# Performance work log

Measured on AMD Instinct MI355X. Metric: run time of the kernel, lower is better.

Reference implementation:

```python
import jax, jax.numpy as jnp
import numpy as np

DEN_LEAKY = 1e-05
NUM_LEAKY = 1e-20


def _chain_objf(xexp, lengths, e_in, e_out, e_pdf, e_prob, leaky, final, coeff):
    """Leaky-HMM forward recursion (pychain forward_backward objective).

    xexp: [B,T,D] exp'd clamped network outputs
    e_*:  edge lists, either shared [E] or per-utterance [B,E]
    leaky/final: [S] or [B,S]
    Returns scalar objf = sum_b log p(X_b | graph_b).
    """
    B, T, D = xexp.shape
    if leaky.ndim == 1:
        leaky = jnp.broadcast_to(leaky[None, :], (B, leaky.shape[0]))
        final = jnp.broadcast_to(final[None, :], (B, final.shape[0]))
    S = leaky.shape[1]
    if e_in.ndim == 1:
        E = e_in.shape[0]
        e_in = jnp.broadcast_to(e_in[None, :], (B, E))
        e_out = jnp.broadcast_to(e_out[None, :], (B, E))
        e_pdf = jnp.broadcast_to(e_pdf[None, :], (B, E))
        e_prob = jnp.broadcast_to(e_prob[None, :], (B, E))
    seg = (e_out + S * jnp.arange(B, dtype=e_out.dtype)[:, None]).ravel()

    # alpha at t=0: mass 1 on start_state (0), plus leaky mass (alpha_sum = 1)
    alpha0 = jnp.zeros((B, S), xexp.dtype).at[:, 0].set(1.0)
    alpha0 = alpha0 + coeff * leaky

    mask_t = jnp.arange(T)[:, None] < lengths[None, :]  # [T,B] ragged frame mask

    def step(carry, inp):
        alpha, logz = carry
        xt, m = inp  # xt: [B,D], m: [B]
        # transition scores: alpha[src] * graph_prob * exp_logit[pdf]
        vals = (jnp.take_along_axis(alpha, e_in, axis=1)
                * e_prob
                * jnp.take_along_axis(xt, e_pdf, axis=1))  # [B,E]
        anew = jax.ops.segment_sum(vals.ravel(), seg, num_segments=B * S).reshape(B, S)
        asum = anew.sum(-1, keepdims=True)  # [B,1] per-frame arbitrary scale
        adash = (anew + coeff * leaky * asum) / asum  # leaky-HMM + renorm
        alpha = jnp.where(m[:, None], adash, alpha)
        logz = logz + jnp.where(m, jnp.log(asum[:, 0]), 0.0)
        return (alpha, logz), None

    (alpha, logz), _ = jax.lax.scan(
        step, (alpha0, jnp.zeros((B,), xexp.dtype)),
        (jnp.transpose(xexp, (1, 0, 2)), mask_t))
    return jnp.sum(logz + jnp.log(jnp.sum(alpha * final, axis=-1)))


def setup_inputs() -> dict:
    key = jax.random.key(0)
    ks = jax.random.split(key, 12)
    B, T, D = 32, 400, 2048
    S_den, E_den = 2000, 60000
    S_num, E_num = 512, 2048
    x = jax.random.normal(ks[0], (B, T, D), dtype=jnp.float32)
    x_lengths = jnp.clip(T - jnp.arange(B, dtype=jnp.int32) * 8, 32, T)  # sorted desc
    den_e_in = jax.random.randint(ks[1], (E_den,), 0, S_den, dtype=jnp.int32)
    den_e_out = jax.random.randint(ks[2], (E_den,), 0, S_den, dtype=jnp.int32)
    den_e_pdf = jax.random.randint(ks[3], (E_den,), 0, D, dtype=jnp.int32)
    den_e_prob = jax.random.uniform(ks[4], (E_den,), dtype=jnp.float32, minval=0.05, maxval=1.0)
    den_leaky = jax.random.uniform(ks[5], (S_den,), dtype=jnp.float32, minval=0.01, maxval=1.0)
    den_final = jax.random.uniform(ks[6], (S_den,), dtype=jnp.float32, minval=0.1, maxval=1.0)
    num_e_in = jax.random.randint(ks[7], (B, E_num), 0, S_num, dtype=jnp.int32)
    num_e_out = jax.random.randint(ks[8], (B, E_num), 0, S_num, dtype=jnp.int32)
    num_e_pdf = jax.random.randint(ks[9], (B, E_num), 0, D, dtype=jnp.int32)
    num_e_prob = jax.random.uniform(ks[10], (B, E_num), dtype=jnp.float32, minval=0.05, maxval=1.0)
    k11, k12 = jax.random.split(ks[11])
    num_leaky = jax.random.uniform(k11, (B, S_num), dtype=jnp.float32, minval=0.01, maxval=1.0)
    num_final = jax.random.uniform(k12, (B, S_num), dtype=jnp.float32, minval=0.1, maxval=1.0)
    return {"x": x, "x_lengths": x_lengths,
            "den_e_in": den_e_in, "den_e_out": den_e_out, "den_e_pdf": den_e_pdf,
            "den_e_prob": den_e_prob, "den_leaky": den_leaky, "den_final": den_final,
            "num_e_in": num_e_in, "num_e_out": num_e_out, "num_e_pdf": num_e_pdf,
            "num_e_prob": num_e_prob, "num_leaky": num_leaky, "num_final": num_final}


def reference(x, x_lengths, den_e_in, den_e_out, den_e_pdf, den_e_prob, den_leaky,
              den_final, num_e_in, num_e_out, num_e_pdf, num_e_prob, num_leaky,
              num_final):
    xexp = jnp.exp(jnp.clip(x, -30.0, 30.0))
    den_objf = _chain_objf(xexp, x_lengths, den_e_in, den_e_out, den_e_pdf,
                           den_e_prob, den_leaky, den_final, DEN_LEAKY)
    num_objf = _chain_objf(xexp, x_lengths, num_e_in, num_e_out, num_e_pdf,
                           num_e_prob, num_leaky, num_final, NUM_LEAKY)
    objf = -(num_objf - den_objf)
    return objf / x_lengths.sum().astype(x.dtype)
```

## Files before the change

kernel.cpp:

```cpp
#include <hip/hip_runtime.h>
#include <math.h>

#define B_SZ   32
#define T_SZ   400
#define D_SZ   2048
#define S_DEN  2000
#define E_DEN  60000
#define S_NUM  512
#define E_NUM  2048
#define DEN_C  1e-5f
#define NUM_C  1e-20f

#define P_CH   8
#define NTHR   512
#define EPT    16
#define EPC    8192

#define REC_OFF     0u
#define ANEWG_OFF   0u
#define PACK_OFF    960000u
#define ROWPTR_OFF  1484288u
#define CNT_OFF     1492352u
#define CUR_OFF     1500352u
#define SROW_OFF    1508352u
#define RSPLIT_OFF  1524736u
#define PSUM_OFF    1524800u
#define CTR_OFF     1528896u
#define XCD_OFF     1530944u
#define TOTD_OFF    1531968u
#define TOTN_OFF    1532096u
#define WS_BYTES    1532224u

__device__ __forceinline__ float expclip(float v) {
    return __expf(fminf(fmaxf(v, -30.f), 30.f));
}
__device__ __forceinline__ float ldf_agent(const float* p) {
    return __hip_atomic_load(p, __ATOMIC_RELAXED, __HIP_MEMORY_SCOPE_AGENT);
}
__device__ __forceinline__ int ldi_agent(const int* p) {
    return __hip_atomic_load(p, __ATOMIC_RELAXED, __HIP_MEMORY_SCOPE_AGENT);
}
__device__ __forceinline__ void stf_agent(float* p, float v) {
    __hip_atomic_store(p, v, __ATOMIC_RELAXED, __HIP_MEMORY_SCOPE_AGENT);
}
__device__ __forceinline__ void sti_agent(int* p, int v) {
    __hip_atomic_store(p, v, __ATOMIC_RELAXED, __HIP_MEMORY_SCOPE_AGENT);
}

__global__ void prep_init(char* ws) {
    int tid = threadIdx.x;
    int* cnt = (int*)(ws + CNT_OFF);
    int* cur = (int*)(ws + CUR_OFF);
    for (int i = tid; i < S_DEN; i += 256) { cnt[i] = 0; cur[i] = 0; }
    int* ctr = (int*)(ws + CTR_OFF);
    for (int i = tid; i < B_SZ * 16; i += 256) ctr[i] = 0;
    int* xcd = (int*)(ws + XCD_OFF);
    if (tid < B_SZ * 8) xcd[tid] = 0;
}

__global__ void prep_hist(const int* __restrict__ e_out, char* ws) {
    int e = blockIdx.x * blockDim.x + threadIdx.x;
    if (e < E_DEN) atomicAdd((int*)(ws + CNT_OFF) + e_out[e], 1);
}

__global__ __launch_bounds__(1024) void prep_scan(char* ws) {
    __shared__ int sb[2][2048];
    const int* cnt = (const int*)(ws + CNT_OFF);
    int* rowp = (int*)(ws + ROWPTR_OFF);
    int tid = threadIdx.x;
    for (int i = tid; i < 2048; i += 1024) sb[0][i] = (i < S_DEN) ? cnt[i] : 0;
    __syncthreads();
    int cur = 0;
    for (int d = 1; d < 2048; d <<= 1) {
        for (int i = tid; i < 2048; i += 1024)
            sb[1 - cur][i] = sb[cur][i] + ((i >= d) ? sb[cur][i - d] : 0);
        __syncthreads();
        cur ^= 1;
    }
    if (tid == 0) rowp[0] = 0;
    for (int i = tid; i < S_DEN; i += 1024) rowp[i + 1] = sb[cur][i];
    __syncthreads();
    if (tid == 0) {
        int* rs = (int*)(ws + RSPLIT_OFF);
        rs[0] = 0; rs[P_CH] = S_DEN;
        for (int p = 1; p < P_CH; ++p) {
            int target = (E_DEN / P_CH) * p;
            int lo = 0, hi = S_DEN;
            while (lo < hi) {
                int mid = (lo + hi) >> 1;
                int v = (mid == 0) ? 0 : sb[cur][mid - 1];
                if (v >= target) hi = mid; else lo = mid + 1;
            }
            rs[p] = lo;
        }
    }
}

__global__ void prep_scatter(const int* __restrict__ e_in, const int* __restrict__ e_out,
                             const int* __restrict__ e_pdf, const float* __restrict__ e_prob,
                             char* ws) {
    int e = blockIdx.x * blockDim.x + threadIdx.x;
    if (e >= E_DEN) return;
    const int* rowp = (const int*)(ws + ROWPTR_OFF);
    int* cur = (int*)(ws + CUR_OFF);
    int4* recs = (int4*)(ws + REC_OFF);
    int o = e_out[e];
    int pos = rowp[o] + atomicAdd(&cur[o], 1);
    int4 r;
    r.x = e_in[e]; r.y = e_pdf[e];
    r.z = __float_as_int(e_prob[e]);
    r.w = o;
    recs[pos] = r;
}

__global__ void prep_pack(char* ws) {
    int slot = blockIdx.x * blockDim.x + threadIdx.x;
    if (slot >= P_CH * EPC) return;
    int p = slot >> 13;
    int k = slot & (EPC - 1);
    const int* rowp = (const int*)(ws + ROWPTR_OFF);
    const int* rs = (const int*)(ws + RSPLIT_OFF);
    int ebase = rowp[rs[p]], eend = rowp[rs[p + 1]];
    uint2* pk = (uint2*)(ws + PACK_OFF);
    int idx = ebase + k;
    uint2 val;
    int myrow;
    if (idx < eend) {
        const int4* r4 = (const int4*)(ws + REC_OFF);
        int4 r = r4[idx];
        myrow = r.w;
        int nxt = (idx + 1 < eend) ? r4[idx + 1].w : myrow;
        unsigned d = (unsigned)(nxt - myrow);
        if (d > 1023u) d = 1023u;
        val = make_uint2((unsigned)r.x | ((unsigned)r.y << 11) | (d << 22),
                         (unsigned)r.z);
    } else {
        val = make_uint2(0u, 0u);
        myrow = rs[p];
    }
    pk[slot] = val;
    if ((k & (EPT - 1)) == 0)
        ((int*)(ws + SROW_OFF))[(p << 9) + (k >> 4)] = myrow;
}

__global__ __launch_bounds__(NTHR, 2) void chain_fwd6(
    const float* __restrict__ x, const int* __restrict__ lengths,
    const float* __restrict__ den_leaky, const float* __restrict__ den_final,
    const int* __restrict__ num_in, const int* __restrict__ num_out,
    const int* __restrict__ num_pdf, const float* __restrict__ num_prob,
    const float* __restrict__ num_leaky, const float* __restrict__ num_final,
    char* __restrict__ ws)
{
    __shared__ float alpha[2048];
    __shared__ float xrow[2048];
    __shared__ float anew[2048];
    __shared__ float nalpha[S_NUM];
    __shared__ float nanew[S_NUM];
    __shared__ float red[24];
    __shared__ int sSame;
    extern __shared__ float dynpad[];
    const int tid = threadIdx.x;
    if (lengths[0] == -12345) dynpad[tid] = 1.f;

    const int b = blockIdx.x & (B_SZ - 1);
    const int p = blockIdx.x >> 5;
    const bool isNum = (p == 0);
    const int len = lengths[b];
    const float* xb = x + (size_t)b * T_SZ * D_SZ;
    const int* rs = (const int*)(ws + RSPLIT_OFF);
    const int rlo = rs[p], rhi = rs[p + 1];
    float* anewg = (float*)(ws + ANEWG_OFF) + ((size_t)(b << 1) << 11);
    float* psumg = (float*)(ws + PSUM_OFF);
    int* ctr = (int*)(ws + CTR_OFF) + (b << 4);
    int* xcdArr = (int*)(ws + XCD_OFF);

    int myxcc = 0;
    asm volatile("s_getreg_b32 %0, hwreg(HW_REG_XCC_ID)" : "=s"(myxcc));
    if (tid == 0) {
        sti_agent(&xcdArr[(b << 3) + p], myxcc + 1);
        asm volatile("s_waitcnt vmcnt(0)" ::: "memory");
        __hip_atomic_fetch_add(ctr + 1, 1, __ATOMIC_RELAXED, __HIP_MEMORY_SCOPE_AGENT);
    }
    if (tid < 64) {
        int gd = 0;
        while (ldi_agent(ctr + 1) < P_CH) {
            __builtin_amdgcn_s_sleep(2);
            if (++gd > (1 << 16)) break;
        }
        int v = (tid < 8) ? ldi_agent(&xcdArr[(b << 3) + tid]) : -1;
        int v0 = __shfl(v, 0, 64);
        bool eq = (tid < 8) ? (v == v0 && v != 0) : true;
        unsigned long long m = __ballot(eq);
        if (tid == 0) sSame = (~m == 0ULL) ? 1 : 0;
    }

    float lc[4], fc[4];
    #pragma unroll
    for (int i = 0; i < 4; ++i) {
        int s = tid + (i << 9);
        lc[i] = (s < S_DEN) ? DEN_C * den_leaky[s] : 0.f;
        fc[i] = (s < S_DEN) ? den_final[s] : 0.f;
    }
    #pragma unroll
    for (int i = 0; i < 4; ++i) {
        int s = tid + (i << 9);
        alpha[s] = lc[i] + ((s == 0) ? 1.f : 0.f);
        anew[s] = 0.f;
        xrow[s] = expclip(xb[s]);
    }

    float nlk = 0.f, nfn = 0.f, nlogz = 0.f;
    int nein[4], neout[4], nepdf[4]; float neprb[4];
    if (isNum) {
        nlk = num_leaky[(b << 9) + tid];
        nfn = num_final[(b << 9) + tid];
        #pragma unroll
        for (int k = 0; k < 4; ++k) {
            int e = (b << 11) + tid + (k << 9);
            nein[k] = num_in[e]; neout[k] = num_out[e];
            nepdf[k] = num_pdf[e]; neprb[k] = num_prob[e];
        }
        nalpha[tid] = NUM_C * nlk + ((tid == 0) ? 1.f : 0.f);
        nanew[tid] = 0.f;
    }

    const uint4* __restrict__ pk4 = (const uint4*)(ws + PACK_OFF);
    const int qb = (p << 12) + (tid << 3);
    const uint4 c0 = pk4[qb + 0], c1 = pk4[qb + 1], c2 = pk4[qb + 2], c3 = pk4[qb + 3];
    const uint4 c4 = pk4[qb + 4], c5 = pk4[qb + 5], c6 = pk4[qb + 6], c7 = pk4[qb + 7];
    const int row0 = ((const int*)(ws + SROW_OFF))[(p << 9) + tid];
    float logz = 0.f;
    __syncthreads();
    const bool fastSt = (sSame != 0);

    for (int t = 0; t < len; ++t) {
        const int par = t & 1;
        const int tn = (t + 1 < len) ? t + 1 : t;
        const float* xq = xb + (size_t)tn * D_SZ;
        const float xn0 = xq[tid], xn1 = xq[tid + 512];
        const float xn2 = xq[tid + 1024], xn3 = xq[tid + 1536];

        float acc = 0.f, psum = 0.f;
        int row = row0;
        {
            const unsigned w[16] = {c0.x, c0.z, c1.x, c1.z, c2.x, c2.z, c3.x, c3.z,
                                    c4.x, c4.z, c5.x, c5.z, c6.x, c6.z, c7.x, c7.z};
            const unsigned pr[16] = {c0.y, c0.w, c1.y, c1.w, c2.y, c2.w, c3.y, c3.w,
                                     c4.y, c4.w, c5.y, c5.w, c6.y, c6.w, c7.y, c7.w};
            float av[16], xv[16];
            #pragma unroll
            for (int i = 0; i < 16; ++i) av[i] = alpha[w[i] & 2047u];
            #pragma unroll
            for (int i = 0; i < 16; ++i) xv[i] = xrow[(w[i] >> 11) & 2047u];
            #pragma unroll
            for (int i = 0; i < 16; ++i) {
                acc = __fmaf_rn(av[i] * __uint_as_float(pr[i]), xv[i], acc);
                const unsigned d = w[i] >> 22;
                if (d) { psum += acc; atomicAdd(&anew[row], acc); acc = 0.f; row += (int)d; }
            }
        }
        psum += acc;
        if (acc != 0.f) atomicAdd(&anew[row], acc);
        #pragma unroll
        for (int o = 32; o > 0; o >>= 1) psum += __shfl_down(psum, o, 64);
        if ((tid & 63) == 0) red[tid >> 6] = psum;
        __syncthreads();

        float* ag = anewg + (par << 11);
        const int pidx = ((b << 1) | par) << 4;
        if (tid == 0) {
            float bs = red[0]+red[1]+red[2]+red[3]+red[4]+red[5]+red[6]+red[7];
            if (fastSt) psumg[pidx + p] = bs;
            else        stf_agent(&psumg[pidx + p], bs);
        }
        if (fastSt) {
            for (int r = rlo + tid; r < rhi; r += NTHR) { ag[r] = anew[r]; anew[r] = 0.f; }
        } else {
            for (int r = rlo + tid; r < rhi; r += NTHR) { stf_agent(&ag[r], anew[r]); anew[r] = 0.f; }
        }
        asm volatile("s_waitcnt vmcnt(0)" ::: "memory");
        if ((tid & 63) == 0)
            __hip_atomic_fetch_add(ctr, 1, __ATOMIC_RELAXED, __HIP_MEMORY_SCOPE_AGENT);

        if (isNum) {
            #pragma unroll
            for (int k = 0; k < 4; ++k) {
                float v = nalpha[nein[k]] * neprb[k] * xrow[nepdf[k]];
                atomicAdd(&nanew[neout[k]], v);
            }
            __syncthreads();
            float ps = nanew[tid];
            #pragma unroll
            for (int o = 32; o > 0; o >>= 1) ps += __shfl_down(ps, o, 64);
            if ((tid & 63) == 0) red[8 + (tid >> 6)] = ps;
        }

        xrow[tid]        = expclip(xn0);
        xrow[tid + 512]  = expclip(xn1);
        xrow[tid + 1024] = expclip(xn2);
        xrow[tid + 1536] = expclip(xn3);

        if (tid < 64) {
            const int target = (P_CH * (NTHR / 64)) * (t + 1);
            int gd = 0;
            while (ldi_agent(ctr) < target) {
                __builtin_amdgcn_s_sleep(1);
                if (++gd > (1 << 15)) break;
            }
            if (tid < 8) red[16 + tid] = ldf_agent(&psumg[pidx + tid]);
        }
        __syncthreads();

        const float asum = red[16]+red[17]+red[18]+red[19]
                         + red[20]+red[21]+red[22]+red[23];
        const float inv = 1.f / asum;
        #pragma unroll
        for (int i = 0; i < 4; ++i) {
            const int s = tid + (i << 9);
            float an = (s < S_DEN) ? ldf_agent(&ag[s]) : 0.f;
            alpha[s] = __fmaf_rn(an, inv, lc[i]);
        }
        logz += logf(asum);
        if (isNum) {
            const float nasum = red[8]+red[9]+red[10]+red[11]
                              + red[12]+red[13]+red[14]+red[15];
            nalpha[tid] = __fmaf_rn(NUM_C * nlk, nasum, nanew[tid]) * (1.f / nasum);
            nanew[tid] = 0.f;
            nlogz += logf(nasum);
        }
        __syncthreads();
    }

    if (isNum) {
        float fs = alpha[tid] * fc[0] + alpha[tid + 512] * fc[1]
                 + alpha[tid + 1024] * fc[2] + alpha[tid + 1536] * fc[3];
        #pragma unroll
        for (int o = 32; o > 0; o >>= 1) fs += __shfl_down(fs, o, 64);
        if ((tid & 63) == 0) red[tid >> 6] = fs;
        __syncthreads();
        if (tid == 0) {
            float tot = red[0]+red[1]+red[2]+red[3]+red[4]+red[5]+red[6]+red[7];
            ((float*)(ws + TOTD_OFF))[b] = logz + logf(tot);
        }
        __syncthreads();
        float nfs = nalpha[tid] * nfn;
        #pragma unroll
        for (int o = 32; o > 0; o >>= 1) nfs += __shfl_down(nfs, o, 64);
        if ((tid & 63) == 0) red[tid >> 6] = nfs;
        __syncthreads();
        if (tid == 0) {
            float tot = red[0]+red[1]+red[2]+red[3]+red[4]+red[5]+red[6]+red[7];
            ((float*)(ws + TOTN_OFF))[b] = nlogz + logf(tot);
        }
    }
}

__global__ void combine2(const char* __restrict__ ws, const int* __restrict__ lengths,
                         float* __restrict__ out) {
    const float* totd = (const float*)(ws + TOTD_OFF);
    const float* totn = (const float*)(ws + TOTN_OFF);
    int tid = threadIdx.x;
    float v = 0.f, l = 0.f;
    if (tid < B_SZ) { v = totd[tid] - totn[tid]; l = (float)lengths[tid]; }
    #pragma unroll
    for (int o = 32; o > 0; o >>= 1) { v += __shfl_down(v, o, 64); l += __shfl_down(l, o, 64); }
    if (tid == 0) out[0] = v / l;
}

__global__ __launch_bounds__(1024) void chain_fwd_kernel(
    const float* __restrict__ x, const int* __restrict__ lengths,
    const int* __restrict__ den_in, const int* __restrict__ den_out,
    const int* __restrict__ den_pdf, const float* __restrict__ den_prob,
    const float* __restrict__ den_leaky, const float* __restrict__ den_final,
    const int* __restrict__ num_in, const int* __restrict__ num_out,
    const int* __restrict__ num_pdf, const float* __restrict__ num_prob,
    const float* __restrict__ num_leaky, const float* __restrict__ num_final,
    float* __restrict__ part)
{
    __shared__ float xrow[D_SZ];
    __shared__ float alpha[S_DEN];
    __shared__ float anew[S_DEN];
    __shared__ float red[17];
    const int tid = threadIdx.x;
    const int nthr = 1024;
    const bool is_den = blockIdx.x < B_SZ;
    const int b = blockIdx.x & (B_SZ - 1);
    int S, E;
    const int *e_in, *e_out, *e_pdf;
    const float *e_prob, *leaky, *fin;
    float coeff;
    if (is_den) {
        S = S_DEN; E = E_DEN;
        e_in = den_in; e_out = den_out; e_pdf = den_pdf; e_prob = den_prob;
        leaky = den_leaky; fin = den_final; coeff = DEN_C;
    } else {
        S = S_NUM; E = E_NUM;
        e_in = num_in + b * E_NUM; e_out = num_out + b * E_NUM;
        e_pdf = num_pdf + b * E_NUM; e_prob = num_prob + b * E_NUM;
        leaky = num_leaky + b * S_NUM; fin = num_final + b * S_NUM;
        coeff = NUM_C;
    }
    const int len = lengths[b];
    const float* xb = x + (size_t)b * T_SZ * D_SZ;
    for (int s = tid; s < S; s += nthr)
        alpha[s] = coeff * leaky[s] + (s == 0 ? 1.0f : 0.0f);
    float logz = 0.0f;
    for (int t = 0; t < len; ++t) {
        for (int s = tid; s < S; s += nthr) anew[s] = 0.0f;
        const float* xt = xb + (size_t)t * D_SZ;
        for (int d = tid; d < D_SZ; d += nthr)
            xrow[d] = __expf(fminf(fmaxf(xt[d], -30.0f), 30.0f));
        __syncthreads();
        for (int e = tid; e < E; e += nthr) {
            float v = alpha[e_in[e]] * e_prob[e] * xrow[e_pdf[e]];
            atomicAdd(&anew[e_out[e]], v);
        }
        __syncthreads();
        float ps = 0.0f;
        for (int s = tid; s < S; s += nthr) ps += anew[s];
        #pragma unroll
        for (int off = 32; off > 0; off >>= 1) ps += __shfl_down(ps, off, 64);
        if ((tid & 63) == 0) red[tid >> 6] = ps;
        __syncthreads();
        if (tid < 64) {
            float v = (tid < 16) ? red[tid] : 0.0f;
            #pragma unroll
            for (int off = 8; off > 0; off >>= 1) v += __shfl_down(v, off, 64);
            if (tid == 0) red[16] = v;
        }
        __syncthreads();
        const float asum = red[16];
        const float inv = 1.0f / asum;
        for (int s = tid; s < S; s += nthr)
            alpha[s] = (anew[s] + coeff * leaky[s] * asum) * inv;
        logz += logf(asum);
        __syncthreads();
    }
    float fs = 0.0f;
    for (int s = tid; s < S; s += nthr) fs += alpha[s] * fin[s];
    #pragma unroll
    for (int off = 32; off > 0; off >>= 1) fs += __shfl_down(fs, off, 64);
    if ((tid & 63) == 0) red[tid >> 6] = fs;
    __syncthreads();
    if (tid < 64) {
        float v = (tid < 16) ? red[tid] : 0.0f;
        #pragma unroll
        for (int off = 8; off > 0; off >>= 1) v += __shfl_down(v, off, 64);
        if (tid == 0) part[blockIdx.x] = logz + logf(v);
    }
}

__global__ void combine_kernel(const float* __restrict__ part,
                               const int* __restrict__ lengths,
                               float* __restrict__ out)
{
    int tid = threadIdx.x;
    float v = 0.0f, l = 0.0f;
    if (tid < B_SZ) { v = part[tid] - part[B_SZ + tid]; l = (float)lengths[tid]; }
    #pragma unroll
    for (int off = 32; off > 0; off >>= 1) { v += __shfl_down(v, off, 64); l += __shfl_down(l, off, 64); }
    if (tid == 0) out[0] = v / l;
}

extern "C" void kernel_launch(void* const* d_in, const int* in_sizes, int n_in,
                              void* d_out, int out_size, void* d_ws, size_t ws_size,
                              hipStream_t stream)
{
    const float* x          = (const float*)d_in[0];
    const int*   lengths    = (const int*)  d_in[1];
    const int*   den_in_p   = (const int*)  d_in[2];
    const int*   den_out_p  = (const int*)  d_in[3];
    const int*   den_pdf_p  = (const int*)  d_in[4];
    const float* den_prob_p = (const float*)d_in[5];
    const float* den_leaky  = (const float*)d_in[6];
    const float* den_final  = (const float*)d_in[7];
    const int*   num_in_p   = (const int*)  d_in[8];
    const int*   num_out_p  = (const int*)  d_in[9];
    const int*   num_pdf_p  = (const int*)  d_in[10];
    const float* num_prob_p = (const float*)d_in[11];
    const float* num_leaky  = (const float*)d_in[12];
    const float* num_final  = (const float*)d_in[13];

    if (ws_size >= WS_BYTES) {
        char* ws = (char*)d_ws;
        hipLaunchKernelGGL(prep_init, dim3(1), dim3(256), 0, stream, ws);
        hipLaunchKernelGGL(prep_hist, dim3((E_DEN + 255) / 256), dim3(256), 0, stream,
                           den_out_p, ws);
        hipLaunchKernelGGL(prep_scan, dim3(1), dim3(1024), 0, stream, ws);
        hipLaunchKernelGGL(prep_scatter, dim3((E_DEN + 255) / 256), dim3(256), 0, stream,
                           den_in_p, den_out_p, den_pdf_p, den_prob_p, ws);
        hipLaunchKernelGGL(prep_pack, dim3((P_CH * EPC + 255) / 256), dim3(256), 0, stream, ws);
        hipLaunchKernelGGL(chain_fwd6, dim3(P_CH * B_SZ), dim3(NTHR), 57344, stream,
                           x, lengths, den_leaky, den_final,
                           num_in_p, num_out_p, num_pdf_p, num_prob_p,
                           num_leaky, num_final, ws);
        hipLaunchKernelGGL(combine2, dim3(1), dim3(64), 0, stream,
                           ws, lengths, (float*)d_out);
    } else {
        float* part = (float*)d_ws;
        hipLaunchKernelGGL(chain_fwd_kernel, dim3(2 * B_SZ), dim3(1024), 0, stream,
                           x, lengths,
                           den_in_p, den_out_p, den_pdf_p, den_prob_p, den_leaky, den_final,
                           num_in_p, num_out_p, num_pdf_p, num_prob_p, num_leaky, num_final,
                           part);
        hipLaunchKernelGGL(combine_kernel, dim3(1), dim3(64), 0, stream,
                           part, lengths, (float*)d_out);
    }
}
```

Measured before the change: 2.710 ms.

## Replace global per-batch counter barrier with per-chunk flags and wave-local row gathers

Each block now publishes a per-chunk progress flag once all its waves have stored their anew rows, instead of every wave incrementing one shared global counter. Each wave then waits only on the flag of the chunk whose rows it gathers, loads those rows and computes their partial sum. The frame sum therefore comes from the gathered alpha values, and the separate per-block psum exchange goes away. The leaky term moves to a shared array, and the dynamic shared padding shrinks to keep occupancy the same. This cuts contention on the global atomic and overlaps the waits across waves, at the cost of more complex synchronisation and a wave-to-chunk mapping that relies on eight waves matching eight chunks.

```diff
diff --git a/kernel.cpp b/kernel.cpp
--- a/kernel.cpp
+++ b/kernel.cpp
@@ -24,12 +24,12 @@
 #define CUR_OFF     1500352u
 #define SROW_OFF    1508352u
 #define RSPLIT_OFF  1524736u
-#define PSUM_OFF    1524800u
-#define CTR_OFF     1528896u
-#define XCD_OFF     1530944u
-#define TOTD_OFF    1531968u
-#define TOTN_OFF    1532096u
-#define WS_BYTES    1532224u
+#define FLAG_OFF    1524800u
+#define CTR_OFF     1541184u
+#define XCD_OFF     1543232u
+#define TOTD_OFF    1544256u
+#define TOTN_OFF    1544384u
+#define WS_BYTES    1544512u
 
 __device__ __forceinline__ float expclip(float v) {
     return __expf(fminf(fmaxf(v, -30.f), 30.f));
@@ -52,6 +52,8 @@
     int* cnt = (int*)(ws + CNT_OFF);
     int* cur = (int*)(ws + CUR_OFF);
     for (int i = tid; i < S_DEN; i += 256) { cnt[i] = 0; cur[i] = 0; }
+    int* flags = (int*)(ws + FLAG_OFF);
+    for (int i = tid; i < B_SZ * 8 * 16; i += 256) flags[i] = 0;
     int* ctr = (int*)(ws + CTR_OFF);
     for (int i = tid; i < B_SZ * 16; i += 256) ctr[i] = 0;
     int* xcd = (int*)(ws + XCD_OFF);
@@ -143,7 +145,7 @@
         ((int*)(ws + SROW_OFF))[(p << 9) + (k >> 4)] = myrow;
 }
 
-__global__ __launch_bounds__(NTHR, 2) void chain_fwd6(
+__global__ __launch_bounds__(NTHR, 2) void chain_fwd7(
     const float* __restrict__ x, const int* __restrict__ lengths,
     const float* __restrict__ den_leaky, const float* __restrict__ den_final,
     const int* __restrict__ num_in, const int* __restrict__ num_out,
@@ -154,12 +156,16 @@
     __shared__ float alpha[2048];
     __shared__ float xrow[2048];
     __shared__ float anew[2048];
+    __shared__ float slc[2048];
     __shared__ float nalpha[S_NUM];
     __shared__ float nanew[S_NUM];
-    __shared__ float red[24];
-    __shared__ int sSame;
+    __shared__ float red[16];
+    __shared__ int   lcnt;
+    __shared__ int   sSame;
     extern __shared__ float dynpad[];
     const int tid = threadIdx.x;
+    const int wid = tid >> 6;
+    const int lane = tid & 63;
     if (lengths[0] == -12345) dynpad[tid] = 1.f;
 
     const int b = blockIdx.x & (B_SZ - 1);
@@ -169,10 +175,15 @@
     const float* xb = x + (size_t)b * T_SZ * D_SZ;
     const int* rs = (const int*)(ws + RSPLIT_OFF);
     const int rlo = rs[p], rhi = rs[p + 1];
+    const int rloW = rs[wid], rhiW = rs[wid + 1];
     float* anewg = (float*)(ws + ANEWG_OFF) + ((size_t)(b << 1) << 11);
-    float* psumg = (float*)(ws + PSUM_OFF);
+    int* flags = (int*)(ws + FLAG_OFF);
     int* ctr = (int*)(ws + CTR_OFF) + (b << 4);
     int* xcdArr = (int*)(ws + XCD_OFF);
+    int* myflag = &flags[((b << 3) + p) << 4];
+    int* wflag  = &flags[((b << 3) + wid) << 4];
+
+    if (tid == 0) lcnt = 0;
 
     int myxcc = 0;
     asm volatile("s_getreg_b32 %0, hwreg(HW_REG_XCC_ID)" : "=s"(myxcc));
@@ -194,17 +205,14 @@
         if (tid == 0) sSame = (~m == 0ULL) ? 1 : 0;
     }
 
-    float lc[4], fc[4];
+    float fc[4];
     #pragma unroll
     for (int i = 0; i < 4; ++i) {
         int s = tid + (i << 9);
-        lc[i] = (s < S_DEN) ? DEN_C * den_leaky[s] : 0.f;
+        float lv = (s < S_DEN) ? DEN_C * den_leaky[s] : 0.f;
+        slc[s] = lv;
         fc[i] = (s < S_DEN) ? den_final[s] : 0.f;
-    }
-    #pragma unroll
-    for (int i = 0; i < 4; ++i) {
-        int s = tid + (i << 9);
-        alpha[s] = lc[i] + ((s == 0) ? 1.f : 0.f);
+        alpha[s] = lv + ((s == 0) ? 1.f : 0.f);
         anew[s] = 0.f;
         xrow[s] = expclip(xb[s]);
     }
@@ -240,7 +248,7 @@
         const float xn0 = xq[tid], xn1 = xq[tid + 512];
         const float xn2 = xq[tid + 1024], xn3 = xq[tid + 1536];
 
-        float acc = 0.f, psum = 0.f;
+        float acc = 0.f;
         int row = row0;
         {
             const unsigned w[16] = {c0.x, c0.z, c1.x, c1.z, c2.x, c2.z, c3.x, c3.z,
@@ -256,31 +264,23 @@
             for (int i = 0; i < 16; ++i) {
                 acc = __fmaf_rn(av[i] * __uint_as_float(pr[i]), xv[i], acc);
                 const unsigned d = w[i] >> 22;
-                if (d) { psum += acc; atomicAdd(&anew[row], acc); acc = 0.f; row += (int)d; }
+                if (d) { atomicAdd(&anew[row], acc); acc = 0.f; row += (int)d; }
             }
         }
-        psum += acc;
         if (acc != 0.f) atomicAdd(&anew[row], acc);
-        #pragma unroll
-        for (int o = 32; o > 0; o >>= 1) psum += __shfl_down(psum, o, 64);
-        if ((tid & 63) == 0) red[tid >> 6] = psum;
         __syncthreads();
 
         float* ag = anewg + (par << 11);
-        const int pidx = ((b << 1) | par) << 4;
-        if (tid == 0) {
-            float bs = red[0]+red[1]+red[2]+red[3]+red[4]+red[5]+red[6]+red[7];
-            if (fastSt) psumg[pidx + p] = bs;
-            else        stf_agent(&psumg[pidx + p], bs);
-        }
         if (fastSt) {
             for (int r = rlo + tid; r < rhi; r += NTHR) { ag[r] = anew[r]; anew[r] = 0.f; }
         } else {
             for (int r = rlo + tid; r < rhi; r += NTHR) { stf_agent(&ag[r], anew[r]); anew[r] = 0.f; }
         }
         asm volatile("s_waitcnt vmcnt(0)" ::: "memory");
-        if ((tid & 63) == 0)
-            __hip_atomic_fetch_add(ctr, 1, __ATOMIC_RELAXED, __HIP_MEMORY_SCOPE_AGENT);
+        if (lane == 0) {
+            int old = atomicAdd(&lcnt, 1);
+            if (old == 8 * t + 7) sti_agent(myflag, t + 1);
+        }
 
         if (isNum) {
             #pragma unroll
@@ -292,7 +292,7 @@
             float ps = nanew[tid];
             #pragma unroll
             for (int o = 32; o > 0; o >>= 1) ps += __shfl_down(ps, o, 64);
-            if ((tid & 63) == 0) red[8 + (tid >> 6)] = ps;
+            if (lane == 0) red[8 + wid] = ps;
         }
 
         xrow[tid]        = expclip(xn0);
@@ -300,25 +300,30 @@
         xrow[tid + 1024] = expclip(xn2);
         xrow[tid + 1536] = expclip(xn3);
 
-        if (tid < 64) {
-            const int target = (P_CH * (NTHR / 64)) * (t + 1);
+        {
             int gd = 0;
-            while (ldi_agent(ctr) < target) {
+            while (ldi_agent(wflag) < t + 1) {
                 __builtin_amdgcn_s_sleep(1);
                 if (++gd > (1 << 15)) break;
             }
-            if (tid < 8) red[16 + tid] = ldf_agent(&psumg[pidx + tid]);
-        }
-        __syncthreads();
-
-        const float asum = red[16]+red[17]+red[18]+red[19]
-                         + red[20]+red[21]+red[22]+red[23];
+            float wsum = 0.f;
+            for (int r = rloW + lane; r < rhiW; r += 64) {
+                float an = ldf_agent(&ag[r]);
+                alpha[r] = an;
+                wsum += an;
+            }
+            #pragma unroll
+            for (int o = 32; o > 0; o >>= 1) wsum += __shfl_down(wsum, o, 64);
+            if (lane == 0) red[wid] = wsum;
+        }
+        __syncthreads();
+
+        const float asum = red[0]+red[1]+red[2]+red[3]+red[4]+red[5]+red[6]+red[7];
         const float inv = 1.f / asum;
         #pragma unroll
         for (int i = 0; i < 4; ++i) {
             const int s = tid + (i << 9);
-            float an = (s < S_DEN) ? ldf_agent(&ag[s]) : 0.f;
-            alpha[s] = __fmaf_rn(an, inv, lc[i]);
+            alpha[s] = __fmaf_rn(alpha[s], inv, slc[s]);
         }
         logz += logf(asum);
         if (isNum) {
@@ -336,7 +341,7 @@
                  + alpha[tid + 1024] * fc[2] + alpha[tid + 1536] * fc[3];
         #pragma unroll
         for (int o = 32; o > 0; o >>= 1) fs += __shfl_down(fs, o, 64);
-        if ((tid & 63) == 0) red[tid >> 6] = fs;
+        if (lane == 0) red[wid] = fs;
         __syncthreads();
         if (tid == 0) {
             float tot = red[0]+red[1]+red[2]+red[3]+red[4]+red[5]+red[6]+red[7];
@@ -346,7 +351,7 @@
         float nfs = nalpha[tid] * nfn;
         #pragma unroll
         for (int o = 32; o > 0; o >>= 1) nfs += __shfl_down(nfs, o, 64);
-        if ((tid & 63) == 0) red[tid >> 6] = nfs;
+        if (lane == 0) red[wid] = nfs;
         __syncthreads();
         if (tid == 0) {
             float tot = red[0]+red[1]+red[2]+red[3]+red[4]+red[5]+red[6]+red[7];
@@ -490,7 +495,7 @@
         hipLaunchKernelGGL(prep_scatter, dim3((E_DEN + 255) / 256), dim3(256), 0, stream,
                            den_in_p, den_out_p, den_pdf_p, den_prob_p, ws);
         hipLaunchKernelGGL(prep_pack, dim3((P_CH * EPC + 255) / 256), dim3(256), 0, stream, ws);
-        hipLaunchKernelGGL(chain_fwd6, dim3(P_CH * B_SZ), dim3(NTHR), 57344, stream,
+        hipLaunchKernelGGL(chain_fwd7, dim3(P_CH * B_SZ), dim3(NTHR), 46080, stream,
                            x, lengths, den_leaky, den_final,
                            num_in_p, num_out_p, num_pdf_p, num_prob_p,
                            num_leaky, num_final, ws);
```

Measured after the change: 2.801 ms. 3.3% more time.
